# Kernel tuning notes

Hardware: AMD Instinct MI355X
Metric: run time of the kernel (lower is better)

Reference implementation:

```python
import jax, jax.numpy as jnp
import numpy as np

N, E, H, S, F = 50000, 800000, 96, 48, 24


def _mlp(x, W1, b1, W2, b2):
    # equinox MLP depth=1: Linear -> relu -> Linear (identity final activation)
    h = jax.nn.relu(x @ W1.T + b1)
    return h @ W2.T + b2


def _segment_softmax(scores, seg, num_segments):
    mx = jax.ops.segment_max(scores, seg, num_segments=num_segments)
    e = jnp.exp(scores - mx[seg])
    s = jax.ops.segment_sum(e, seg, num_segments=num_segments)
    return e / (s[seg] + 1e-9)


def setup_inputs() -> dict:
    key = jax.random.key(0)
    ks = jax.random.split(key, 32)
    def p(i, shape):
        return jax.random.normal(ks[i], shape, dtype=jnp.float32) * 0.05
    in_attn = 2 * H + 2 * S + F   # 312
    w_attn = 2 * H                # 192
    gin = 3 * H                   # 288
    inp = {
        "x": p(0, (N, H)),
        "x_s": p(1, (N, S)),
        "edge_features": p(2, (E, F)),
        "edge_index": jax.random.randint(ks[3], (2, E), 0, N),
        # fwd attention MLP: in_attn -> w_attn -> 1
        "fwd_W1": p(4, (w_attn, in_attn)), "fwd_b1": p(5, (w_attn,)),
        "fwd_W2": p(6, (1, w_attn)), "fwd_b2": p(7, (1,)),
        # rev gate MLP: in_attn -> w_attn -> 1
        "rev_W1": p(8, (w_attn, in_attn)), "rev_b1": p(9, (w_attn,)),
        "rev_W2": p(10, (1, w_attn)), "rev_b2": p(11, (1,)),
        # reset gate MLP: 3H -> 3H -> H
        "reset_W1": p(12, (gin, gin)), "reset_b1": p(13, (gin,)),
        "reset_W2": p(14, (H, gin)), "reset_b2": p(15, (H,)),
        # update gate MLP: 3H -> 3H -> H
        "update_W1": p(16, (gin, gin)), "update_b1": p(17, (gin,)),
        "update_W2": p(18, (H, gin)), "update_b2": p(19, (H,)),
        # candidate MLP: 3H -> 3H -> H
        "cand_W1": p(20, (gin, gin)), "cand_b1": p(21, (gin,)),
        "cand_W2": p(22, (H, gin)), "cand_b2": p(23, (H,)),
    }
    return inp


def reference(x, x_s, edge_features, edge_index,
              fwd_W1, fwd_b1, fwd_W2, fwd_b2,
              rev_W1, rev_b1, rev_W2, rev_b2,
              reset_W1, reset_b1, reset_W2, reset_b2,
              update_W1, update_b1, update_W2, update_b2,
              cand_W1, cand_b1, cand_W2, cand_b2):
    num_nodes = x.shape[0]
    src, dest = edge_index[0], edge_index[1]

    def compute_messages(s, d, W1, b1, W2, b2, use_softmax):
        feat = jnp.concatenate([x[s], x[d], x_s[s], x_s[d], edge_features], axis=-1)
        raw = _mlp(feat, W1, b1, W2, b2)[:, 0]  # [E]
        if use_softmax:
            raw = jax.nn.leaky_relu(raw) / jnp.sqrt(jnp.asarray(x.shape[-1], dtype=x.dtype))
            w = _segment_softmax(raw, d, num_nodes)
        else:
            w = jax.nn.sigmoid(raw)
        agg = jax.ops.segment_sum(x[s] * w[:, None], d, num_segments=num_nodes)
        return agg, w

    fwd_msgs, fwd_w = compute_messages(src, dest, fwd_W1, fwd_b1, fwd_W2, fwd_b2, True)
    rev_msgs, rev_w = compute_messages(dest, src, rev_W1, rev_b1, rev_W2, rev_b2, False)

    messages = jnp.concatenate([fwd_msgs, rev_msgs], axis=-1)  # [N, 2H]
    gate_input = jnp.concatenate([x, messages], axis=-1)        # [N, 3H]
    r_gate = jax.nn.sigmoid(_mlp(gate_input, reset_W1, reset_b1, reset_W2, reset_b2))
    z_gate = jax.nn.sigmoid(_mlp(gate_input, update_W1, update_b1, update_W2, update_b2))
    cand_input = jnp.concatenate([r_gate * x, messages], axis=-1)
    candidate = jnp.tanh(_mlp(cand_input, cand_W1, cand_b1, cand_W2, cand_b2))
    update = (1 - z_gate) * x + z_gate * candidate
    return (update, fwd_w, rev_w, z_gate, r_gate)
```

## Files before the change

### kernel.cpp

```cpp
#include <hip/hip_runtime.h>
#include <math.h>

typedef unsigned short u16;
typedef unsigned int   u32;

#define HDIM 96
#define SDIM 48
#define FDIM 24
#define KA   312
#define WATT 192
#define KG   288

#define KT_A  10
#define KT_G  9
#define NS    296

#define NFRAG (2 * KT_A * 12 * 64)
#define W1F_Q (KT_G * 18 * 64)
#define W2F_Q (KT_G * 6 * 64)
#define NODEF_Q (3 * (W1F_Q + W2F_Q))

#define PB_EDGE 60
#define PB_W1   41
#define PB_W2   14
#define PB_NODE (3 * (PB_W1 + PB_W2))

typedef __attribute__((ext_vector_type(8))) __bf16 bf16x8;
typedef __attribute__((ext_vector_type(4))) float  f32x4;

__device__ __forceinline__ u16 f2bf(float f) {
  u32 u = __float_as_uint(f);
  u = (u + 0x7FFFu + ((u >> 16) & 1u)) >> 16;
  return (u16)u;
}
__device__ __forceinline__ float bf2f(u16 v) {
  return __uint_as_float((u32)v << 16);
}
__device__ __forceinline__ u32 pack2(float a, float b) {
  return (u32)f2bf(a) | ((u32)f2bf(b) << 16);
}
__device__ __forceinline__ f32x4 mfma_bf16(bf16x8 a, bf16x8 b, f32x4 c) {
  return __builtin_amdgcn_mfma_f32_16x16x32_bf16(a, b, c, 0, 0, 0);
}

__global__ __launch_bounds__(256) void prep_all(
    const float* __restrict__ fW1, const float* __restrict__ rW1,
    uint4* __restrict__ Bfrag,
    const float* __restrict__ W1r, const float* __restrict__ W2r,
    const float* __restrict__ W1u, const float* __restrict__ W2u,
    const float* __restrict__ W1c, const float* __restrict__ W2c,
    uint4* __restrict__ NodeF,
    const float* __restrict__ x, const float* __restrict__ xs,
    u32* __restrict__ xb, u32* __restrict__ xsb, int N)
{
  int b = blockIdx.x;
  const int tid = threadIdx.x;

  if (b < PB_EDGE) {
    const int idx = b * 256 + tid;
    const int lane = idx & 63;
    const int frag = idx >> 6;
    const int nt   = frag % 12;
    const int rest = frag / 12;
    const int kt   = rest % KT_A;
    const int mlp  = rest / KT_A;
    const int q = lane >> 4, c = lane & 15;
    const int n  = nt * 16 + c;
    const int p0 = kt * 16 + q * 4;
    const float* W = mlp ? rW1 : fW1;
    u32 v[4];
#pragma unroll
    for (int w = 0; w < 4; ++w) {
      const int p = p0 + w;
      u32 val = 0u;
      if (p < 156) {
        int src = p;
        if (mlp) {
          if (src < 48)       src += 48;
          else if (src < 96)  src -= 48;
          else if (src < 120) src += 24;
          else if (src < 144) src -= 24;
        }
        const float2 wv = *(const float2*)(W + (size_t)n * KA + 2 * src);
        val = pack2(wv.x, wv.y);
      }
      v[w] = val;
    }
    Bfrag[idx] = make_uint4(v[0], v[1], v[2], v[3]);
    return;
  }
  b -= PB_EDGE;

  if (b < PB_NODE) {
    const int mlp = b / (PB_W1 + PB_W2);
    const int lb  = b % (PB_W1 + PB_W2);
    const float* W;
    uint4* o;
    int NT, idx;
    if (lb < PB_W1) {
      NT = 18; idx = lb * 256 + tid;
      W = (mlp == 0) ? W1r : (mlp == 1) ? W1u : W1c;
      o = NodeF + (size_t)mlp * (W1F_Q + W2F_Q);
    } else {
      NT = 6; idx = (lb - PB_W1) * 256 + tid;
      W = (mlp == 0) ? W2r : (mlp == 1) ? W2u : W2c;
      o = NodeF + (size_t)mlp * (W1F_Q + W2F_Q) + W1F_Q;
    }
    if (idx >= KT_G * NT * 64) return;
    const int lane = idx & 63;
    const int frag = idx >> 6;
    const int nt = frag % NT, kt = frag / NT;
    const int q = lane >> 4, c = lane & 15;
    const int n = nt * 16 + c;
    const int k0 = kt * 32 + q * 8;
    u32 v[4];
#pragma unroll
    for (int w = 0; w < 4; ++w) {
      const float2 wv = *(const float2*)(W + (size_t)n * KG + k0 + 2 * w);
      v[w] = pack2(wv.x, wv.y);
    }
    o[idx] = make_uint4(v[0], v[1], v[2], v[3]);
    return;
  }
  b -= PB_NODE;

  {
    const int i = b * 256 + tid;
    const int nx = N * 48;
    if (i < nx) {
      const float2 v = ((const float2*)x)[i];
      xb[i] = pack2(v.x, v.y);
    } else if (i < nx + N * 24) {
      const float2 v = ((const float2*)xs)[i - nx];
      xsb[i - nx] = pack2(v.x, v.y);
    }
  }
}

__global__ __launch_bounds__(512, 4) void edge_kernel(
    const u32* __restrict__ xb, const u32* __restrict__ xsb,
    const float* __restrict__ ef, const int* __restrict__ ei,
    const u16* __restrict__ Bfrag,
    const float* __restrict__ fb1, const float* __restrict__ fW2,
    const float* __restrict__ fb2,
    const float* __restrict__ rb1, const float* __restrict__ rW2,
    const float* __restrict__ rb2,
    float* __restrict__ pe, float* __restrict__ out_revw, int N, int E)
{
  __shared__ float red[2][4][64];

  const int tid  = threadIdx.x;
  const int wave = tid >> 6, lane = tid & 63;
  const int mlp  = wave >> 2;
  const int w4   = wave & 3;
  const int q = lane >> 4, c = lane & 15;
  const int e0 = blockIdx.x * 64;

  int em[4], sm[4], dm[4];
#pragma unroll
  for (int m = 0; m < 4; ++m) {
    em[m] = min(e0 + m * 16 + c, E - 1);
    int s = ei[em[m]], d = ei[(size_t)E + em[m]];
    sm[m] = min(max(s, 0), N - 1);
    dm[m] = min(max(d, 0), N - 1);
  }

  const bf16x8* __restrict__ Bf = (const bf16x8*)Bfrag;

  f32x4 acc[4][3];
#pragma unroll
  for (int m = 0; m < 4; ++m)
    for (int t = 0; t < 3; ++t)
      acc[m][t] = (f32x4){0.f, 0.f, 0.f, 0.f};

#pragma unroll
  for (int kt = 0; kt < KT_A; ++kt) {
    const int p0 = kt * 16 + q * 4;
    bf16x8 a[4];
#pragma unroll
    for (int m = 0; m < 4; ++m) {
      uint4 av;
      if (kt < 3) {
        av = *(const uint4*)(xb + (size_t)sm[m] * 48 + p0);
      } else if (kt < 6) {
        av = *(const uint4*)(xb + (size_t)dm[m] * 48 + (p0 - 48));
      } else if (kt == 6) {
        av = *(const uint4*)(xsb + (size_t)sm[m] * 24 + (p0 - 96));
      } else if (kt == 7) {
        const u32* p = (q < 2) ? xsb + (size_t)sm[m] * 24 + (p0 - 96)
                               : xsb + (size_t)dm[m] * 24 + (p0 - 120);
        av = *(const uint4*)p;
      } else if (kt == 8) {
        av = *(const uint4*)(xsb + (size_t)dm[m] * 24 + (p0 - 120));
      } else {
        if (q < 3) {
          const float* efp = ef + (size_t)em[m] * 24 + (p0 - 144) * 2;
          const float4 f0 = *(const float4*)efp;
          const float4 f1 = *(const float4*)(efp + 4);
          av = make_uint4(pack2(f0.x, f0.y), pack2(f0.z, f0.w),
                          pack2(f1.x, f1.y), pack2(f1.z, f1.w));
        } else {
          av = make_uint4(0u, 0u, 0u, 0u);
        }
      }
      a[m] = __builtin_bit_cast(bf16x8, av);
    }
#pragma unroll
    for (int t = 0; t < 3; ++t) {
      const bf16x8 b = Bf[(((mlp * KT_A + kt) * 12) + w4 * 3 + t) * 64 + lane];
#pragma unroll
      for (int m = 0; m < 4; ++m)
        acc[m][t] = mfma_bf16(a[m], b, acc[m][t]);
    }
  }

  const float* b1p = mlp ? rb1 : fb1;
  const float* W2p = mlp ? rW2 : fW2;
  float p[4][4];
#pragma unroll
  for (int m = 0; m < 4; ++m)
    for (int r = 0; r < 4; ++r) p[m][r] = 0.f;
#pragma unroll
  for (int t = 0; t < 3; ++t) {
    const int n = (w4 * 3 + t) * 16 + c;
    const float b1f = b1p[n];
    const float w2f = W2p[n];
#pragma unroll
    for (int m = 0; m < 4; ++m)
      for (int r = 0; r < 4; ++r) {
        float h = acc[m][t][r] + b1f;
        h = h > 0.f ? h : 0.f;
        p[m][r] += h * w2f;
      }
  }
  for (int off = 1; off <= 8; off <<= 1)
#pragma unroll
    for (int m = 0; m < 4; ++m)
      for (int r = 0; r < 4; ++r)
        p[m][r] += __shfl_xor(p[m][r], off, 64);

  if (c == 0) {
#pragma unroll
    for (int m = 0; m < 4; ++m)
      for (int r = 0; r < 4; ++r)
        red[mlp][w4][m * 16 + q * 4 + r] = p[m][r];
  }
  __syncthreads();

  if (tid < 64 && e0 + tid < E) {
    const int e = e0 + tid;
    float rawf = red[0][0][tid] + red[0][1][tid] + red[0][2][tid] + red[0][3][tid];
    rawf += fb2[0];
    const float lr = rawf > 0.f ? rawf : 0.01f * rawf;
    pe[e] = __expf(lr * 0.10206207261596575f);
    float rawr = red[1][0][tid] + red[1][1][tid] + red[1][2][tid] + red[1][3][tid];
    rawr += rb2[0];
    out_revw[e] = 1.f / (1.f + __expf(-rawr));
  }
}

__global__ __launch_bounds__(256) void k_hist(
    const int* __restrict__ ei, int* __restrict__ deg_d,
    int* __restrict__ deg_s, int N, int E)
{
  const int e = blockIdx.x * 256 + threadIdx.x;
  if (e >= E) return;
  const int s = min(max(ei[e], 0), N - 1);
  const int d = min(max(ei[(size_t)E + e], 0), N - 1);
  atomicAdd(&deg_d[d], 1);
  atomicAdd(&deg_s[s], 1);
}

__global__ __launch_bounds__(256) void k_scan1(
    const int* __restrict__ deg_d, const int* __restrict__ deg_s,
    int* __restrict__ start_d, int* __restrict__ start_s,
    int* __restrict__ bsum_d, int* __restrict__ bsum_s, int N)
{
  __shared__ int sh[256];
  const int t = threadIdx.x, i = blockIdx.x * 256 + t;
  {
    const int v = (i < N) ? deg_d[i] : 0;
    sh[t] = v; __syncthreads();
    for (int off = 1; off < 256; off <<= 1) {
      const int u = (t >= off) ? sh[t - off] : 0;
      __syncthreads();
      sh[t] += u;
      __syncthreads();
    }
    if (i < N) start_d[i] = sh[t] - v;
    if (t == 255) bsum_d[blockIdx.x] = sh[255];
    __syncthreads();
  }
  {
    const int v = (i < N) ? deg_s[i] : 0;
    sh[t] = v; __syncthreads();
    for (int off = 1; off < 256; off <<= 1) {
      const int u = (t >= off) ? sh[t - off] : 0;
      __syncthreads();
      sh[t] += u;
      __syncthreads();
    }
    if (i < N) start_s[i] = sh[t] - v;
    if (t == 255) bsum_s[blockIdx.x] = sh[255];
  }
}

__global__ __launch_bounds__(256) void k_scan3(
    int* __restrict__ start_d, int* __restrict__ start_s,
    const int* __restrict__ bsum_d, const int* __restrict__ bsum_s,
    int* __restrict__ pos_d, int* __restrict__ pos_s, int N)
{
  __shared__ int offs[2];
  const int t = threadIdx.x;
  if (t < 2) {
    const int* bs = t ? bsum_s : bsum_d;
    int r = 0;
    for (int bb = 0; bb < (int)blockIdx.x; ++bb) r += bs[bb];
    offs[t] = r;
  }
  __syncthreads();
  const int i = blockIdx.x * 256 + t;
  if (i >= N) return;
  const int vd = start_d[i] + offs[0]; start_d[i] = vd; pos_d[i] = vd;
  const int vs = start_s[i] + offs[1]; start_s[i] = vs; pos_s[i] = vs;
}

__global__ __launch_bounds__(256) void k_fill(
    const int* __restrict__ ei, int* __restrict__ pos_d,
    int* __restrict__ pos_s, int* __restrict__ eidx_d,
    int* __restrict__ eidx_s, int N, int E)
{
  const int e = blockIdx.x * 256 + threadIdx.x;
  if (e >= E) return;
  const int s = min(max(ei[e], 0), N - 1);
  const int d = min(max(ei[(size_t)E + e], 0), N - 1);
  eidx_d[atomicAdd(&pos_d[d], 1)] = e;
  eidx_s[atomicAdd(&pos_s[s], 1)] = e;
}

__global__ __launch_bounds__(256) void k_agg_all(
    const float* __restrict__ x, const int* __restrict__ ei,
    const float* __restrict__ pe, const float* __restrict__ revw,
    const int* __restrict__ start_d, const int* __restrict__ end_d,
    const int* __restrict__ eidx_d,
    const int* __restrict__ start_s, const int* __restrict__ end_s,
    const int* __restrict__ eidx_s,
    u16* __restrict__ fwdm, u16* __restrict__ revm,
    float* __restrict__ out_fwdw, int N, int E, int ablk)
{
  int b = blockIdx.x;
  const int dir = (b >= ablk) ? 1 : 0;
  if (dir) b -= ablk;
  const int g = threadIdx.x >> 5;
  const int l = threadIdx.x & 31;
  const int n = b * 8 + g;
  if (n >= N) return;

  const int* start = dir ? start_s : start_d;
  const int* endp  = dir ? end_s   : end_d;
  const int* eidx  = dir ? eidx_s  : eidx_d;
  const int beg = start[n], end = endp[n];

  float inv = 1.f;
  if (dir == 0) {
    float sum = 0.f;
    for (int i = beg + l; i < end; i += 32) sum += pe[eidx[i]];
    for (int off = 16; off; off >>= 1) sum += __shfl_xor(sum, off, 32);
    inv = 1.f / (sum + 1e-9f);
    for (int i = beg + l; i < end; i += 32) {
      const int e = eidx[i];
      out_fwdw[e] = pe[e] * inv;
    }
  }

  float a0 = 0.f, a1 = 0.f, a2 = 0.f;
  for (int i = beg; i < end; ++i) {
    const int e = eidx[i];
    const float w = (dir == 0) ? pe[e] * inv : revw[e];
    const int o = (dir == 0) ? min(max(ei[e], 0), N - 1)
                             : min(max(ei[(size_t)E + e], 0), N - 1);
    const float* xr = x + (size_t)o * 96;
    a0 += w * xr[l];
    a1 += w * xr[l + 32];
    a2 += w * xr[l + 64];
  }
  u16* orow = (dir ? revm : fwdm) + (size_t)n * 96;
  orow[l] = f2bf(a0); orow[l + 32] = f2bf(a1); orow[l + 64] = f2bf(a2);
}

__device__ __forceinline__ void node_mlp(
    const u16* __restrict__ Alds, u16* __restrict__ Hlds,
    const bf16x8* __restrict__ W1f, const bf16x8* __restrict__ W2f,
    const float* __restrict__ b1,
    int wave, int lane, int q, int c, int ntc, int ntc2,
    f32x4 (&acc2)[4][2])
{
  f32x4 acc[4][5];
#pragma unroll
  for (int m = 0; m < 4; ++m)
    for (int t = 0; t < 5; ++t) acc[m][t] = (f32x4){0.f, 0.f, 0.f, 0.f};

#pragma unroll
  for (int kt = 0; kt < KT_G; ++kt) {
    bf16x8 a[4];
#pragma unroll
    for (int m = 0; m < 4; ++m)
      a[m] = *(const bf16x8*)&Alds[(m * 16 + c) * NS + kt * 32 + q * 8];
#pragma unroll
    for (int t = 0; t < 5; ++t) {
      if (t < ntc) {
        const int nt = wave + 4 * t;
        const bf16x8 b = W1f[(kt * 18 + nt) * 64 + lane];
#pragma unroll
        for (int m = 0; m < 4; ++m)
          acc[m][t] = mfma_bf16(a[m], b, acc[m][t]);
      }
    }
  }

  __syncthreads();
#pragma unroll
  for (int t = 0; t < 5; ++t) {
    if (t < ntc) {
      const int n = (wave + 4 * t) * 16 + c;
      const float b1f = b1[n];
#pragma unroll
      for (int m = 0; m < 4; ++m)
        for (int r = 0; r < 4; ++r) {
          float h = acc[m][t][r] + b1f;
          h = h > 0.f ? h : 0.f;
          Hlds[(m * 16 + q * 4 + r) * NS + n] = f2bf(h);
        }
    }
  }
  __syncthreads();

#pragma unroll
  for (int m = 0; m < 4; ++m)
    for (int t = 0; t < 2; ++t) acc2[m][t] = (f32x4){0.f, 0.f, 0.f, 0.f};
#pragma unroll
  for (int kt = 0; kt < KT_G; ++kt) {
    bf16x8 a[4];
#pragma unroll
    for (int m = 0; m < 4; ++m)
      a[m] = *(const bf16x8*)&Hlds[(m * 16 + c) * NS + kt * 32 + q * 8];
#pragma unroll
    for (int t = 0; t < 2; ++t) {
      if (t < ntc2) {
        const int nt = wave + 4 * t;
        const bf16x8 b = W2f[(kt * 6 + nt) * 64 + lane];
#pragma unroll
        for (int m = 0; m < 4; ++m)
          acc2[m][t] = mfma_bf16(a[m], b, acc2[m][t]);
      }
    }
  }
}

__global__ __launch_bounds__(256, 2) void node_fused(
    const float* __restrict__ x, const u32* __restrict__ xb,
    const u32* __restrict__ fwdmb, const u32* __restrict__ revmb,
    const uint4* __restrict__ NodeF,
    const float* __restrict__ b1r, const float* __restrict__ b2r,
    const float* __restrict__ b1u, const float* __restrict__ b2u,
    const float* __restrict__ b1c, const float* __restrict__ b2c,
    float* __restrict__ out_r, float* __restrict__ out_z,
    float* __restrict__ out_upd, int N)
{
  __shared__ __align__(16) u16 Alds[64 * NS];
  __shared__ __align__(16) u16 Hlds[64 * NS];

  const int tid = threadIdx.x;
  const int wave = tid >> 6, lane = tid & 63;
  const int q = lane >> 4, c = lane & 15;
  const int n0 = blockIdx.x * 64;
  const int ntc  = (wave < 2) ? 5 : 4;
  const int ntc2 = (wave < 2) ? 2 : 1;

  {
    const int nl = tid >> 2, sub = tid & 3;
    const int node = min(n0 + nl, N - 1);
    const uint4* xr = (const uint4*)(xb    + (size_t)node * 48);
    const uint4* fr = (const uint4*)(fwdmb + (size_t)node * 48);
    const uint4* rr = (const uint4*)(revmb + (size_t)node * 48);
    uint4* Arow = (uint4*)&Alds[nl * NS];
    if (sub == 0) {
      uint4 t0 = xr[0], t1 = xr[1], t2 = xr[2], t3 = xr[3], t4 = xr[4],
            t5 = xr[5], t6 = xr[6], t7 = xr[7], t8 = xr[8];
      Arow[0] = t0; Arow[1] = t1; Arow[2] = t2; Arow[3] = t3; Arow[4] = t4;
      Arow[5] = t5; Arow[6] = t6; Arow[7] = t7; Arow[8] = t8;
    } else if (sub == 1) {
      uint4 t0 = xr[9], t1 = xr[10], t2 = xr[11], t3 = fr[0], t4 = fr[1],
            t5 = fr[2], t6 = fr[3], t7 = fr[4], t8 = fr[5];
      Arow[9] = t0; Arow[10] = t1; Arow[11] = t2; Arow[12] = t3;
      Arow[13] = t4; Arow[14] = t5; Arow[15] = t6; Arow[16] = t7;
      Arow[17] = t8;
    } else if (sub == 2) {
      uint4 t0 = fr[6], t1 = fr[7], t2 = fr[8], t3 = fr[9], t4 = fr[10],
            t5 = fr[11], t6 = rr[0], t7 = rr[1], t8 = rr[2];
      Arow[18] = t0; Arow[19] = t1; Arow[20] = t2; Arow[21] = t3;
      Arow[22] = t4; Arow[23] = t5; Arow[24] = t6; Arow[25] = t7;
      Arow[26] = t8;
    } else {
      uint4 t0 = rr[3], t1 = rr[4], t2 = rr[5], t3 = rr[6], t4 = rr[7],
            t5 = rr[8], t6 = rr[9], t7 = rr[10], t8 = rr[11];
      Arow[27] = t0; Arow[28] = t1; Arow[29] = t2; Arow[30] = t3;
      Arow[31] = t4; Arow[32] = t5; Arow[33] = t6; Arow[34] = t7;
      Arow[35] = t8;
    }
  }
  __syncthreads();

  const bf16x8* W1fr = (const bf16x8*)(NodeF);
  const bf16x8* W2fr = (const bf16x8*)(NodeF + W1F_Q);
  const bf16x8* W1fu = (const bf16x8*)(NodeF + W1F_Q + W2F_Q);
  const bf16x8* W2fu = (const bf16x8*)(NodeF + 2 * W1F_Q + W2F_Q);
  const bf16x8* W1fc = (const bf16x8*)(NodeF + 2 * (W1F_Q + W2F_Q));
  const bf16x8* W2fc = (const bf16x8*)(NodeF + 3 * W1F_Q + 2 * W2F_Q);

  f32x4 acc2[4][2];

  node_mlp(Alds, Hlds, W1fr, W2fr, b1r, wave, lane, q, c, ntc, ntc2, acc2);
  float r_reg[2][4][4];
#pragma unroll
  for (int t = 0; t < 2; ++t) {
    if (t < ntc2) {
      const int n2 = (wave + 4 * t) * 16 + c;
      const float b2f = b2r[n2];
#pragma unroll
      for (int m = 0; m < 4; ++m)
        for (int r = 0; r < 4; ++r) {
          const float v = acc2[m][t][r] + b2f;
          const float rv = 1.f / (1.f + __expf(-v));
          r_reg[t][m][r] = rv;
          const int node = n0 + m * 16 + q * 4 + r;
          if (node < N) out_r[(size_t)node * HDIM + n2] = rv;
        }
    }
  }

  node_mlp(Alds, Hlds, W1fu, W2fu, b1u, wave, lane, q, c, ntc, ntc2, acc2);
  float z_reg[2][4][4];
#pragma unroll
  for (int t = 0; t < 2; ++t) {
    if (t < ntc2) {
      const int n2 = (wave + 4 * t) * 16 + c;
      const float b2f = b2u[n2];
#pragma unroll
      for (int m = 0; m < 4; ++m)
        for (int r = 0; r < 4; ++r) {
          const float v = acc2[m][t][r] + b2f;
          const float zv = 1.f / (1.f + __expf(-v));
          z_reg[t][m][r] = zv;
          const int node = n0 + m * 16 + q * 4 + r;
          if (node < N) out_z[(size_t)node * HDIM + n2] = zv;
        }
    }
  }

#pragma unroll
  for (int t = 0; t < 2; ++t) {
    if (t < ntc2) {
      const int n2 = (wave + 4 * t) * 16 + c;
#pragma unroll
      for (int m = 0; m < 4; ++m)
        for (int r = 0; r < 4; ++r) {
          const int row = m * 16 + q * 4 + r;
          const int idx = row * NS + n2;
          Alds[idx] = f2bf(bf2f(Alds[idx]) * r_reg[t][m][r]);
        }
    }
  }
  __syncthreads();

  node_mlp(Alds, Hlds, W1fc, W2fc, b1c, wave, lane, q, c, ntc, ntc2, acc2);
#pragma unroll
  for (int t = 0; t < 2; ++t) {
    if (t < ntc2) {
      const int n2 = (wave + 4 * t) * 16 + c;
      const float b2f = b2c[n2];
#pragma unroll
      for (int m = 0; m < 4; ++m)
        for (int r = 0; r < 4; ++r) {
          const int node = n0 + m * 16 + q * 4 + r;
          if (node < N) {
            const float v = acc2[m][t][r] + b2f;
            const float ct = tanhf(v);
            const float z = z_reg[t][m][r];
            const float xv = x[(size_t)node * HDIM + n2];
            out_upd[(size_t)node * HDIM + n2] = (1.f - z) * xv + z * ct;
          }
        }
    }
  }
}

__global__ void sentinel_kernel(float* out, int n, float val) {
  const int i = blockIdx.x * 256 + threadIdx.x;
  if (i < n) out[i] = val;
}

extern "C" void kernel_launch(void* const* d_in, const int* in_sizes, int n_in,
                              void* d_out, int out_size, void* d_ws, size_t ws_size,
                              hipStream_t stream) {
  const float* x  = (const float*)d_in[0];
  const float* xs = (const float*)d_in[1];
  const float* ef = (const float*)d_in[2];
  const int*   ei = (const int*)d_in[3];

  const int N = in_sizes[0] / HDIM;
  const int E = in_sizes[3] / 2;

  float* out = (float*)d_out;

  const int NB = (N + 255) / 256;

  const bool sizes_ok =
      n_in == 24 && NB <= 1024 &&
      in_sizes[0] == N * HDIM && in_sizes[1] == N * SDIM &&
      in_sizes[2] == E * FDIM && in_sizes[3] == 2 * E &&
      in_sizes[4] == WATT * KA && in_sizes[5] == WATT &&
      in_sizes[6] == WATT && in_sizes[7] == 1 &&
      in_sizes[12] == KG * KG && in_sizes[13] == KG &&
      in_sizes[14] == HDIM * KG && in_sizes[15] == HDIM &&
      out_size == 3 * N * HDIM + 2 * E;
  if (!sizes_ok) {
    sentinel_kernel<<<(out_size + 255) / 256, 256, 0, stream>>>(out, out_size, 777.0f);
    return;
  }

  const size_t eA = ((size_t)E + 3) & ~(size_t)3;
  const size_t needed =
      (eA + (size_t)NFRAG * 4 + (size_t)NODEF_Q * 4 +
       (size_t)N * 48 + (size_t)N * 24 + 2 * (size_t)N * 48 +
       6 * (size_t)N + 2048 + 2 * (size_t)E) * 4;
  if (ws_size < needed) {
    sentinel_kernel<<<(out_size + 255) / 256, 256, 0, stream>>>(out, out_size, 12345.0f);
    return;
  }
  float* pe    = (float*)d_ws;
  uint4* Bfrag = (uint4*)((u32*)d_ws + eA);
  uint4* NodeF = Bfrag + NFRAG;
  u32*   xbw   = (u32*)(NodeF + NODEF_Q);
  u32*   xsbw  = xbw + (size_t)N * 48;
  u32*   fwdmb = xsbw + (size_t)N * 24;
  u32*   revmb = fwdmb + (size_t)N * 48;
  int* deg_d   = (int*)(revmb + (size_t)N * 48);
  int* deg_s   = deg_d + N;
  int* start_d = deg_s + N;
  int* start_s = start_d + N;
  int* pos_d   = start_s + N;
  int* pos_s   = pos_d + N;
  int* bsum_d  = pos_s + N;
  int* bsum_s  = bsum_d + 1024;
  int* eidx_d  = bsum_s + 1024;
  int* eidx_s  = eidx_d + E;

  float* out_update = out;
  float* out_fwdw   = out + (size_t)N * HDIM;
  float* out_revw   = out_fwdw + E;
  float* out_z      = out_revw + E;
  float* out_r      = out_z + (size_t)N * HDIM;

  (void)hipMemsetAsync(deg_d, 0, 2 * (size_t)N * sizeof(int), stream);

  const int prep_blocks = PB_EDGE + PB_NODE + (N * 72 + 255) / 256;
  prep_all<<<prep_blocks, 256, 0, stream>>>(
      (const float*)d_in[4], (const float*)d_in[8], Bfrag,
      (const float*)d_in[12], (const float*)d_in[14],
      (const float*)d_in[16], (const float*)d_in[18],
      (const float*)d_in[20], (const float*)d_in[22], NodeF,
      x, xs, xbw, xsbw, N);

  const int eblk = (E + 255) / 256;
  k_hist<<<eblk, 256, 0, stream>>>(ei, deg_d, deg_s, N, E);
  k_scan1<<<NB, 256, 0, stream>>>(deg_d, deg_s, start_d, start_s,
                                  bsum_d, bsum_s, N);
  k_scan3<<<NB, 256, 0, stream>>>(start_d, start_s, bsum_d, bsum_s,
                                  pos_d, pos_s, N);
  k_fill<<<eblk, 256, 0, stream>>>(ei, pos_d, pos_s, eidx_d, eidx_s, N, E);

  edge_kernel<<<(E + 63) / 64, 512, 0, stream>>>(
      xbw, xsbw, ef, ei, (const u16*)Bfrag,
      (const float*)d_in[5], (const float*)d_in[6], (const float*)d_in[7],
      (const float*)d_in[9], (const float*)d_in[10], (const float*)d_in[11],
      pe, out_revw, N, E);

  const int ablk = (N + 7) / 8;
  k_agg_all<<<2 * ablk, 256, 0, stream>>>(
      x, ei, pe, out_revw,
      start_d, pos_d, eidx_d, start_s, pos_s, eidx_s,
      (u16*)fwdmb, (u16*)revmb, out_fwdw, N, E, ablk);

  const int nblk = (N + 63) / 64;
  node_fused<<<nblk, 256, 0, stream>>>(
      x, xbw, fwdmb, revmb, NodeF,
      (const float*)d_in[13], (const float*)d_in[15],
      (const float*)d_in[17], (const float*)d_in[19],
      (const float*)d_in[21], (const float*)d_in[23],
      out_r, out_z, out_update, N);
}
```

Before: 1.115 ms.

## Factor edge MLP first layer into per-node projection tables gathered per edge

The first linear layer of the forward and reverse edge MLPs is split by input block. The node-dependent parts (x and x_s of source and destination) are precomputed once per node by a new MFMA projection kernel into four bf16 tables of width 192. The edge kernel then only runs a small MFMA over the edge features, gathers and sums the two node-table rows, and applies bias, ReLU and the second layer as a dot product. This removes most of the per-edge matmul work, at the cost of a large bf16 table in workspace, random 48-byte gathers from it, and extra bf16 rounding of the partial sums.

After: 932.3 us. 16.4% less time.

```diff
diff --git a/kernel.cpp b/kernel.cpp
--- a/kernel.cpp
+++ b/kernel.cpp
@@ -11,19 +11,24 @@
 #define WATT 192
 #define KG   288
 
-#define KT_A  10
 #define KT_G  9
 #define NS    296
 
-#define NFRAG (2 * KT_A * 12 * 64)
+#define PRJB_Q (4 * 5 * 12 * 64)
+#define EFB_Q  (2 * 12 * 64)
+#define EDGEB_Q (PRJB_Q + EFB_Q)
+
 #define W1F_Q (KT_G * 18 * 64)
 #define W2F_Q (KT_G * 6 * 64)
 #define NODEF_Q (3 * (W1F_Q + W2F_Q))
 
-#define PB_EDGE 60
+#define PB_EDGE 66
 #define PB_W1   41
 #define PB_W2   14
 #define PB_NODE (3 * (PB_W1 + PB_W2))
+
+#define PSTR_EF 40
+#define PSTR_H  200
 
 typedef __attribute__((ext_vector_type(8))) __bf16 bf16x8;
 typedef __attribute__((ext_vector_type(4))) float  f32x4;
@@ -36,6 +41,12 @@
 __device__ __forceinline__ float bf2f(u16 v) {
   return __uint_as_float((u32)v << 16);
 }
+__device__ __forceinline__ float bflo(u32 u) {
+  return __uint_as_float(u << 16);
+}
+__device__ __forceinline__ float bfhi(u32 u) {
+  return __uint_as_float(u & 0xffff0000u);
+}
 __device__ __forceinline__ u32 pack2(float a, float b) {
   return (u32)f2bf(a) | ((u32)f2bf(b) << 16);
 }
@@ -45,7 +56,7 @@
 
 __global__ __launch_bounds__(256) void prep_all(
     const float* __restrict__ fW1, const float* __restrict__ rW1,
-    uint4* __restrict__ Bfrag,
+    uint4* __restrict__ EdgeB,
     const float* __restrict__ W1r, const float* __restrict__ W2r,
     const float* __restrict__ W1u, const float* __restrict__ W2u,
     const float* __restrict__ W1c, const float* __restrict__ W2c,
@@ -59,34 +70,52 @@
   if (b < PB_EDGE) {
     const int idx = b * 256 + tid;
     const int lane = idx & 63;
-    const int frag = idx >> 6;
-    const int nt   = frag % 12;
-    const int rest = frag / 12;
-    const int kt   = rest % KT_A;
-    const int mlp  = rest / KT_A;
     const int q = lane >> 4, c = lane & 15;
-    const int n  = nt * 16 + c;
-    const int p0 = kt * 16 + q * 4;
-    const float* W = mlp ? rW1 : fW1;
-    u32 v[4];
-#pragma unroll
-    for (int w = 0; w < 4; ++w) {
-      const int p = p0 + w;
-      u32 val = 0u;
-      if (p < 156) {
-        int src = p;
-        if (mlp) {
-          if (src < 48)       src += 48;
-          else if (src < 96)  src -= 48;
-          else if (src < 120) src += 24;
-          else if (src < 144) src -= 24;
+    if (idx < PRJB_Q) {
+      const int frag = idx >> 6;
+      const int nt   = frag % 12;
+      const int rest = frag / 12;
+      const int kt   = rest % 5;
+      const int tbl  = rest / 5;
+      const float* W = (tbl < 2) ? fW1 : rW1;
+      const int role = tbl & 1;
+      const int n  = nt * 16 + c;
+      const int p0 = kt * 16 + q * 4;
+      u32 v[4];
+#pragma unroll
+      for (int w = 0; w < 4; ++w) {
+        const int p = p0 + w;
+        u32 val = 0u;
+        int col = -1;
+        if (p < 48)      col = role * 96 + 2 * p;
+        else if (p < 72) col = 192 + role * 48 + 2 * (p - 48);
+        if (col >= 0) {
+          const float2 wv = *(const float2*)(W + (size_t)n * KA + col);
+          val = pack2(wv.x, wv.y);
         }
-        const float2 wv = *(const float2*)(W + (size_t)n * KA + 2 * src);
-        val = pack2(wv.x, wv.y);
+        v[w] = val;
       }
-      v[w] = val;
-    }
-    Bfrag[idx] = make_uint4(v[0], v[1], v[2], v[3]);
+      EdgeB[idx] = make_uint4(v[0], v[1], v[2], v[3]);
+    } else {
+      const int i2 = idx - PRJB_Q;
+      const int f2 = i2 >> 6;
+      const int nt = f2 % 12, mlp = f2 / 12;
+      const float* W = mlp ? rW1 : fW1;
+      const int n  = nt * 16 + c;
+      const int p0 = q * 4;
+      u32 v[4];
+#pragma unroll
+      for (int w = 0; w < 4; ++w) {
+        const int p = p0 + w;
+        u32 val = 0u;
+        if (p < 12) {
+          const float2 wv = *(const float2*)(W + (size_t)n * KA + 288 + 2 * p);
+          val = pack2(wv.x, wv.y);
+        }
+        v[w] = val;
+      }
+      EdgeB[idx] = make_uint4(v[0], v[1], v[2], v[3]);
+    }
     return;
   }
   b -= PB_EDGE;
@@ -137,124 +166,185 @@
   }
 }
 
-__global__ __launch_bounds__(512, 4) void edge_kernel(
+__global__ __launch_bounds__(512) void proj_kernel(
     const u32* __restrict__ xb, const u32* __restrict__ xsb,
+    const u16* __restrict__ EdgeB, u16* __restrict__ tabs, int N)
+{
+  const int tid = threadIdx.x;
+  const int wave = tid >> 6, lane = tid & 63;
+  const int q = lane >> 4, c = lane & 15;
+  const int tbl = wave & 3, half = wave >> 2;
+  const int n0 = blockIdx.x * 64;
+
+  int nd[4];
+#pragma unroll
+  for (int m = 0; m < 4; ++m) nd[m] = min(n0 + m * 16 + c, N - 1);
+
+  const bf16x8* __restrict__ Bf = (const bf16x8*)EdgeB;
+
+  f32x4 acc[4][6];
+#pragma unroll
+  for (int m = 0; m < 4; ++m)
+    for (int t = 0; t < 6; ++t) acc[m][t] = (f32x4){0.f, 0.f, 0.f, 0.f};
+
+#pragma unroll
+  for (int kt = 0; kt < 5; ++kt) {
+    bf16x8 a[4];
+#pragma unroll
+    for (int m = 0; m < 4; ++m) {
+      uint4 av;
+      if (kt < 3) {
+        av = *(const uint4*)(xb + (size_t)nd[m] * 48 + kt * 16 + q * 4);
+      } else if (kt == 3) {
+        av = *(const uint4*)(xsb + (size_t)nd[m] * 24 + q * 4);
+      } else {
+        if (q < 2) av = *(const uint4*)(xsb + (size_t)nd[m] * 24 + 16 + q * 4);
+        else       av = make_uint4(0u, 0u, 0u, 0u);
+      }
+      a[m] = __builtin_bit_cast(bf16x8, av);
+    }
+#pragma unroll
+    for (int t = 0; t < 6; ++t) {
+      const int nt = half * 6 + t;
+      const bf16x8 bfr = Bf[(((tbl * 5 + kt) * 12) + nt) * 64 + lane];
+#pragma unroll
+      for (int m = 0; m < 4; ++m)
+        acc[m][t] = mfma_bf16(a[m], bfr, acc[m][t]);
+    }
+  }
+
+  u16* Tp = tabs + (size_t)tbl * N * 192;
+#pragma unroll
+  for (int t = 0; t < 6; ++t) {
+    const int col = (half * 6 + t) * 16 + c;
+#pragma unroll
+    for (int m = 0; m < 4; ++m)
+      for (int r = 0; r < 4; ++r) {
+        const int node = n0 + m * 16 + q * 4 + r;
+        if (node < N) Tp[(size_t)node * 192 + col] = f2bf(acc[m][t][r]);
+      }
+  }
+}
+
+__device__ __forceinline__ float dot24(
+    const u16* __restrict__ Arow, const u16* __restrict__ Brow,
+    const u16* __restrict__ Prow,
+    const float* __restrict__ b1p, const float* __restrict__ w2p)
+{
+  float acc = 0.f;
+  const uint4* A4 = (const uint4*)Arow;
+  const uint4* B4 = (const uint4*)Brow;
+  const uint4* P4 = (const uint4*)Prow;
+  const float4* b14 = (const float4*)b1p;
+  const float4* w24 = (const float4*)w2p;
+#pragma unroll
+  for (int ch = 0; ch < 3; ++ch) {
+    const uint4 aa = A4[ch], bb = B4[ch], pp = P4[ch];
+    const float4 b1a = b14[2 * ch], b1b = b14[2 * ch + 1];
+    const float4 w2a = w24[2 * ch], w2b = w24[2 * ch + 1];
+    const u32 au[4] = {aa.x, aa.y, aa.z, aa.w};
+    const u32 bu[4] = {bb.x, bb.y, bb.z, bb.w};
+    const u32 pu[4] = {pp.x, pp.y, pp.z, pp.w};
+    const float b1s[8] = {b1a.x, b1a.y, b1a.z, b1a.w, b1b.x, b1b.y, b1b.z, b1b.w};
+    const float w2s[8] = {w2a.x, w2a.y, w2a.z, w2a.w, w2b.x, w2b.y, w2b.z, w2b.w};
+#pragma unroll
+    for (int w = 0; w < 4; ++w) {
+      float vL = bflo(au[w]) + bflo(bu[w]) + bflo(pu[w]) + b1s[2 * w];
+      vL = vL > 0.f ? vL : 0.f;
+      acc += vL * w2s[2 * w];
+      float vH = bfhi(au[w]) + bfhi(bu[w]) + bfhi(pu[w]) + b1s[2 * w + 1];
+      vH = vH > 0.f ? vH : 0.f;
+      acc += vH * w2s[2 * w + 1];
+    }
+  }
+  return acc;
+}
+
+__global__ __launch_bounds__(512, 4) void edge_asm(
     const float* __restrict__ ef, const int* __restrict__ ei,
-    const u16* __restrict__ Bfrag,
+    const u16* __restrict__ EdgeB, const u16* __restrict__ tabs,
     const float* __restrict__ fb1, const float* __restrict__ fW2,
     const float* __restrict__ fb2,
     const float* __restrict__ rb1, const float* __restrict__ rW2,
     const float* __restrict__ rb2,
     float* __restrict__ pe, float* __restrict__ out_revw, int N, int E)
 {
-  __shared__ float red[2][4][64];
+  __shared__ __align__(16) u16 EfL[64 * PSTR_EF];
+  __shared__ __align__(16) u16 PefL[2][64 * PSTR_H];
 
   const int tid  = threadIdx.x;
   const int wave = tid >> 6, lane = tid & 63;
-  const int mlp  = wave >> 2;
-  const int w4   = wave & 3;
   const int q = lane >> 4, c = lane & 15;
+  const int mlp = wave >> 2, w4 = wave & 3;
   const int e0 = blockIdx.x * 64;
 
-  int em[4], sm[4], dm[4];
-#pragma unroll
-  for (int m = 0; m < 4; ++m) {
-    em[m] = min(e0 + m * 16 + c, E - 1);
-    int s = ei[em[m]], d = ei[(size_t)E + em[m]];
-    sm[m] = min(max(s, 0), N - 1);
-    dm[m] = min(max(d, 0), N - 1);
-  }
-
-  const bf16x8* __restrict__ Bf = (const bf16x8*)Bfrag;
-
-  f32x4 acc[4][3];
-#pragma unroll
-  for (int m = 0; m < 4; ++m)
-    for (int t = 0; t < 3; ++t)
-      acc[m][t] = (f32x4){0.f, 0.f, 0.f, 0.f};
-
-#pragma unroll
-  for (int kt = 0; kt < KT_A; ++kt) {
-    const int p0 = kt * 16 + q * 4;
+  if (tid < 384) {
+    const int el = tid / 6, part = tid % 6;
+    const int e = min(e0 + el, E - 1);
+    const float4 f = *(const float4*)(ef + (size_t)e * 24 + part * 4);
+    *(uint2*)&EfL[el * PSTR_EF + part * 4] =
+        make_uint2(pack2(f.x, f.y), pack2(f.z, f.w));
+  } else if (tid < 448) {
+    const int el = tid - 384;
+    *(uint4*)&EfL[el * PSTR_EF + 24] = make_uint4(0u, 0u, 0u, 0u);
+  }
+  __syncthreads();
+
+  {
+    const bf16x8* __restrict__ BfAll = (const bf16x8*)EdgeB;
+    f32x4 acc[4][3];
+#pragma unroll
+    for (int m = 0; m < 4; ++m)
+      for (int t = 0; t < 3; ++t) acc[m][t] = (f32x4){0.f, 0.f, 0.f, 0.f};
     bf16x8 a[4];
 #pragma unroll
-    for (int m = 0; m < 4; ++m) {
-      uint4 av;
-      if (kt < 3) {
-        av = *(const uint4*)(xb + (size_t)sm[m] * 48 + p0);
-      } else if (kt < 6) {
-        av = *(const uint4*)(xb + (size_t)dm[m] * 48 + (p0 - 48));
-      } else if (kt == 6) {
-        av = *(const uint4*)(xsb + (size_t)sm[m] * 24 + (p0 - 96));
-      } else if (kt == 7) {
-        const u32* p = (q < 2) ? xsb + (size_t)sm[m] * 24 + (p0 - 96)
-                               : xsb + (size_t)dm[m] * 24 + (p0 - 120);
-        av = *(const uint4*)p;
-      } else if (kt == 8) {
-        av = *(const uint4*)(xsb + (size_t)dm[m] * 24 + (p0 - 120));
-      } else {
-        if (q < 3) {
-          const float* efp = ef + (size_t)em[m] * 24 + (p0 - 144) * 2;
-          const float4 f0 = *(const float4*)efp;
-          const float4 f1 = *(const float4*)(efp + 4);
-          av = make_uint4(pack2(f0.x, f0.y), pack2(f0.z, f0.w),
-                          pack2(f1.x, f1.y), pack2(f1.z, f1.w));
-        } else {
-          av = make_uint4(0u, 0u, 0u, 0u);
-        }
-      }
-      a[m] = __builtin_bit_cast(bf16x8, av);
-    }
+    for (int m = 0; m < 4; ++m)
+      a[m] = *(const bf16x8*)&EfL[(m * 16 + c) * PSTR_EF + q * 8];
 #pragma unroll
     for (int t = 0; t < 3; ++t) {
-      const bf16x8 b = Bf[(((mlp * KT_A + kt) * 12) + w4 * 3 + t) * 64 + lane];
+      const bf16x8 bfr = BfAll[PRJB_Q + ((mlp * 12) + w4 * 3 + t) * 64 + lane];
 #pragma unroll
       for (int m = 0; m < 4; ++m)
-        acc[m][t] = mfma_bf16(a[m], b, acc[m][t]);
-    }
-  }
-
-  const float* b1p = mlp ? rb1 : fb1;
-  const float* W2p = mlp ? rW2 : fW2;
-  float p[4][4];
-#pragma unroll
-  for (int m = 0; m < 4; ++m)
-    for (int r = 0; r < 4; ++r) p[m][r] = 0.f;
-#pragma unroll
-  for (int t = 0; t < 3; ++t) {
-    const int n = (w4 * 3 + t) * 16 + c;
-    const float b1f = b1p[n];
-    const float w2f = W2p[n];
+        acc[m][t] = mfma_bf16(a[m], bfr, acc[m][t]);
+    }
 #pragma unroll
     for (int m = 0; m < 4; ++m)
-      for (int r = 0; r < 4; ++r) {
-        float h = acc[m][t][r] + b1f;
-        h = h > 0.f ? h : 0.f;
-        p[m][r] += h * w2f;
-      }
-  }
-  for (int off = 1; off <= 8; off <<= 1)
-#pragma unroll
-    for (int m = 0; m < 4; ++m)
-      for (int r = 0; r < 4; ++r)
-        p[m][r] += __shfl_xor(p[m][r], off, 64);
-
-  if (c == 0) {
-#pragma unroll
-    for (int m = 0; m < 4; ++m)
-      for (int r = 0; r < 4; ++r)
-        red[mlp][w4][m * 16 + q * 4 + r] = p[m][r];
+      for (int t = 0; t < 3; ++t)
+        for (int r = 0; r < 4; ++r)
+          PefL[mlp][(m * 16 + q * 4 + r) * PSTR_H + (w4 * 3 + t) * 16 + c] =
+              f2bf(acc[m][t][r]);
   }
   __syncthreads();
 
-  if (tid < 64 && e0 + tid < E) {
-    const int e = e0 + tid;
-    float rawf = red[0][0][tid] + red[0][1][tid] + red[0][2][tid] + red[0][3][tid];
-    rawf += fb2[0];
+  const int el = tid >> 3, sub = tid & 7;
+  const int e  = e0 + el;
+  const int ec = min(e, E - 1);
+  int s = ei[ec], d = ei[(size_t)E + ec];
+  s = min(max(s, 0), N - 1);
+  d = min(max(d, 0), N - 1);
+  const int off = sub * 24;
+
+  const u16* Ap0 = tabs;
+  const u16* Bp0 = tabs + (size_t)N * 192;
+  const u16* Ap1 = tabs + 2 * (size_t)N * 192;
+  const u16* Bp1 = tabs + 3 * (size_t)N * 192;
+
+  float accf = dot24(Ap0 + (size_t)s * 192 + off, Bp0 + (size_t)d * 192 + off,
+                     &PefL[0][el * PSTR_H + off], fb1 + off, fW2 + off);
+  float accr = dot24(Ap1 + (size_t)d * 192 + off, Bp1 + (size_t)s * 192 + off,
+                     &PefL[1][el * PSTR_H + off], rb1 + off, rW2 + off);
+
+#pragma unroll
+  for (int o = 1; o <= 4; o <<= 1) {
+    accf += __shfl_xor(accf, o, 64);
+    accr += __shfl_xor(accr, o, 64);
+  }
+
+  if (sub == 0 && e < E) {
+    float rawf = accf + fb2[0];
     const float lr = rawf > 0.f ? rawf : 0.01f * rawf;
     pe[e] = __expf(lr * 0.10206207261596575f);
-    float rawr = red[1][0][tid] + red[1][1][tid] + red[1][2][tid] + red[1][3][tid];
-    rawr += rb2[0];
+    float rawr = accr + rb2[0];
     out_revw[e] = 1.f / (1.f + __expf(-rawr));
   }
 }
@@ -631,21 +721,23 @@
 
   const size_t eA = ((size_t)E + 3) & ~(size_t)3;
   const size_t needed =
-      (eA + (size_t)NFRAG * 4 + (size_t)NODEF_Q * 4 +
+      (eA + (size_t)EDGEB_Q * 4 + (size_t)NODEF_Q * 4 +
        (size_t)N * 48 + (size_t)N * 24 + 2 * (size_t)N * 48 +
-       6 * (size_t)N + 2048 + 2 * (size_t)E) * 4;
+       (size_t)N * 384 + 6 * (size_t)N + 2048 + 2 * (size_t)E) * 4;
   if (ws_size < needed) {
     sentinel_kernel<<<(out_size + 255) / 256, 256, 0, stream>>>(out, out_size, 12345.0f);
     return;
   }
   float* pe    = (float*)d_ws;
-  uint4* Bfrag = (uint4*)((u32*)d_ws + eA);
-  uint4* NodeF = Bfrag + NFRAG;
+  uint4* EdgeB = (uint4*)((u32*)d_ws + eA);
+  uint4* NodeF = EdgeB + EDGEB_Q;
   u32*   xbw   = (u32*)(NodeF + NODEF_Q);
   u32*   xsbw  = xbw + (size_t)N * 48;
   u32*   fwdmb = xsbw + (size_t)N * 24;
   u32*   revmb = fwdmb + (size_t)N * 48;
-  int* deg_d   = (int*)(revmb + (size_t)N * 48);
+  u32*   tabs32 = revmb + (size_t)N * 48;
+  u16*   tabs  = (u16*)tabs32;
+  int* deg_d   = (int*)(tabs32 + (size_t)N * 384);
   int* deg_s   = deg_d + N;
   int* start_d = deg_s + N;
   int* start_s = start_d + N;
@@ -666,7 +758,7 @@
 
   const int prep_blocks = PB_EDGE + PB_NODE + (N * 72 + 255) / 256;
   prep_all<<<prep_blocks, 256, 0, stream>>>(
-      (const float*)d_in[4], (const float*)d_in[8], Bfrag,
+      (const float*)d_in[4], (const float*)d_in[8], EdgeB,
       (const float*)d_in[12], (const float*)d_in[14],
       (const float*)d_in[16], (const float*)d_in[18],
       (const float*)d_in[20], (const float*)d_in[22], NodeF,
@@ -680,8 +772,11 @@
                                   pos_d, pos_s, N);
   k_fill<<<eblk, 256, 0, stream>>>(ei, pos_d, pos_s, eidx_d, eidx_s, N, E);
 
-  edge_kernel<<<(E + 63) / 64, 512, 0, stream>>>(
-      xbw, xsbw, ef, ei, (const u16*)Bfrag,
+  proj_kernel<<<(N + 63) / 64, 512, 0, stream>>>(
+      xbw, xsbw, (const u16*)EdgeB, tabs, N);
+
+  edge_asm<<<(E + 63) / 64, 512, 0, stream>>>(
+      ef, ei, (const u16*)EdgeB, tabs,
       (const float*)d_in[5], (const float*)d_in[6], (const float*)d_in[7],
       (const float*)d_in[9], (const float*)d_in[10], (const float*)d_in[11],
       pe, out_revw, N, E);
```
